# Optimization experiments

Hardware: AMD Instinct MI355X
Metric: run time of the kernel (lower is better)

Reference implementation:

```python
import jax, jax.numpy as jnp
import numpy as np

B, D, K = 8192, 1024, 30


def _sample_neg_indices(key, batch_size, num_negs):
    # per-row uniform indices in [0, 2B) excluding {i, i+B}, matching _sample_negatives
    total = 2 * batch_size
    i = jnp.arange(batch_size)[:, None]                      # [B,1]
    r = jax.random.randint(key, (batch_size, num_negs), 0, total - 2)
    a = r + (r >= i)                                         # skip index i
    b = a + (a >= (i + batch_size))                          # skip index i+B
    return b.astype(jnp.int32)


def setup_inputs() -> dict:
    key = jax.random.key(0)
    k1, k2, k3 = jax.random.split(key, 3)
    return {
        "z_i": jax.random.normal(k1, (B, D), dtype=jnp.float32),
        "z_j": jax.random.normal(k2, (B, D), dtype=jnp.float32),
        "temperature": jnp.asarray(0.2, dtype=jnp.float32),
        "neg_indices": _sample_neg_indices(k3, B, K),        # [B,K] int32
    }


def _l2_normalize(x, eps=1e-12):
    # matches F.normalize(p=2, dim=1): x / max(||x||, eps)
    n = jnp.sqrt(jnp.sum(x * x, axis=1, keepdims=True))
    return x / jnp.maximum(n, eps)


def reference(z_i, z_j, temperature, neg_indices):
    zi = _l2_normalize(z_i)                                  # [B,D]
    zj = _l2_normalize(z_j)                                  # [B,D]
    pos_sim = jnp.sum(zi * zj, axis=1)                       # [B]
    pool = jnp.concatenate([zi, zj], axis=0)                 # [2B,D]
    z_neg = pool[neg_indices]                                # [B,K,D] irregular gather
    neg_sim = jnp.einsum("bd,bkd->bk", zi, z_neg)            # [B,K]
    logits = jnp.concatenate([pos_sim[:, None], neg_sim], axis=1) / temperature  # [B,1+K]
    # cross entropy with labels == 0
    loss = -jnp.mean(jax.nn.log_softmax(logits, axis=1)[:, 0])
    return loss
```

## Files before the change

kernel.cpp:

```cpp
#include <hip/hip_runtime.h>
#include <math.h>

constexpr int NB = 8192;
constexpr int ND = 1024;
constexpr int NK = 30;
constexpr int RS = ND / 4;

#if defined(__has_builtin)
#  if __has_builtin(__builtin_amdgcn_sdot4)
#    define HAVE_SDOT4 1
#  endif
#endif
#ifndef HAVE_SDOT4
#  define HAVE_SDOT4 0
#endif

__device__ __forceinline__ int SDOT4(int a, int b, int acc) {
#if HAVE_SDOT4
    return __builtin_amdgcn_sdot4(a, b, acc, false);
#else
    return acc + (int)(signed char)(a)        * (int)(signed char)(b)
               + (int)(signed char)(a >> 8)   * (int)(signed char)(b >> 8)
               + (int)(signed char)(a >> 16)  * (int)(signed char)(b >> 16)
               + (int)(a >> 24)               * (int)(b >> 24);
#endif
}

__device__ __forceinline__ int pack4_i8(float a, float b, float c, float d) {
    int x0 = (int)rintf(a), x1 = (int)rintf(b), x2 = (int)rintf(c), x3 = (int)rintf(d);
    return (x0 & 255) | ((x1 & 255) << 8) | ((x2 & 255) << 16) | (x3 << 24);
}

__global__ void normalize_i8_kernel(const float* __restrict__ zi,
                                    const float* __restrict__ zj,
                                    int* __restrict__ pool,
                                    int* __restrict__ logits) {
    if (threadIdx.x < 64)
        logits[blockIdx.x * 64 + threadIdx.x] = 0;

    int row  = blockIdx.x * 4 + (threadIdx.x >> 6);
    int lane = threadIdx.x & 63;
    const float* src = (row < NB) ? (zi + (size_t)row * ND)
                                  : (zj + (size_t)(row - NB) * ND);
    float v[16];
    float s = 0.f;
#pragma unroll
    for (int seg = 0; seg < 4; ++seg) {
        float4 t = *reinterpret_cast<const float4*>(src + lane * 16 + seg * 4);
        v[seg * 4 + 0] = t.x; v[seg * 4 + 1] = t.y;
        v[seg * 4 + 2] = t.z; v[seg * 4 + 3] = t.w;
        s += t.x * t.x + t.y * t.y + t.z * t.z + t.w * t.w;
    }
#pragma unroll
    for (int off = 32; off >= 1; off >>= 1)
        s += __shfl_xor(s, off, 64);
    float inv = 127.f / fmaxf(sqrtf(s), 1e-12f);

    int4 w;
    w.x = pack4_i8(v[0]*inv,  v[1]*inv,  v[2]*inv,  v[3]*inv);
    w.y = pack4_i8(v[4]*inv,  v[5]*inv,  v[6]*inv,  v[7]*inv);
    w.z = pack4_i8(v[8]*inv,  v[9]*inv,  v[10]*inv, v[11]*inv);
    w.w = pack4_i8(v[12]*inv, v[13]*inv, v[14]*inv, v[15]*inv);
    *reinterpret_cast<int4*>(pool + (size_t)row * RS + lane * 4) = w;
}

__global__ void loss_chunk_kernel(const int* __restrict__ pool,
                                  const int* __restrict__ neg_idx,
                                  int* __restrict__ logits) {
    int wave = threadIdx.x >> 6;
    int lane = threadIdx.x & 63;
    int c    = blockIdx.x & 7;
    int row  = (blockIdx.x >> 3) * 4 + wave;
    int g    = lane >> 3;
    int p    = lane & 7;

    int myidx = (lane < NK) ? neg_idx[row * NK + lane] : 0;

    const int* cbase = pool + c * 32 + p * 4;
    int4 a4 = *reinterpret_cast<const int4*>(cbase + (size_t)row * RS);

    int4 b4[4];
#pragma unroll
    for (int t = 0; t < 4; ++t) {
        int s = t * 8 + g;
        int r = (s == 0) ? (row + NB)
              : (s < 31) ? __shfl(myidx, s - 1, 64)
                         : 0;
        b4[t] = *reinterpret_cast<const int4*>(cbase + (size_t)r * RS);
    }

    int d0 = 0, d1 = 0, d2 = 0, d3 = 0;
    d0 = SDOT4(a4.x, b4[0].x, d0); d0 = SDOT4(a4.y, b4[0].y, d0);
    d0 = SDOT4(a4.z, b4[0].z, d0); d0 = SDOT4(a4.w, b4[0].w, d0);
    d1 = SDOT4(a4.x, b4[1].x, d1); d1 = SDOT4(a4.y, b4[1].y, d1);
    d1 = SDOT4(a4.z, b4[1].z, d1); d1 = SDOT4(a4.w, b4[1].w, d1);
    d2 = SDOT4(a4.x, b4[2].x, d2); d2 = SDOT4(a4.y, b4[2].y, d2);
    d2 = SDOT4(a4.z, b4[2].z, d2); d2 = SDOT4(a4.w, b4[2].w, d2);
    d3 = SDOT4(a4.x, b4[3].x, d3); d3 = SDOT4(a4.y, b4[3].y, d3);
    d3 = SDOT4(a4.z, b4[3].z, d3); d3 = SDOT4(a4.w, b4[3].w, d3);

#pragma unroll
    for (int off = 1; off <= 4; off <<= 1) {
        d0 += __shfl_xor(d0, off, 64);
        d1 += __shfl_xor(d1, off, 64);
        d2 += __shfl_xor(d2, off, 64);
        d3 += __shfl_xor(d3, off, 64);
    }

    if (p < 4) {
        int val = (p == 0) ? d0 : (p == 1) ? d1 : (p == 2) ? d2 : d3;
        atomicAdd(&logits[row * 32 + p * 8 + g], val);
    }
}

__global__ void lse_kernel(const int* __restrict__ logits,
                           const float* __restrict__ temp_ptr,
                           float* __restrict__ block_part) {
    int wave = threadIdx.x >> 6;
    int lane = threadIdx.x & 63;
    int slot = lane & 31;
    int row  = blockIdx.x * 8 + wave * 2 + (lane >> 5);

    float inv_t = 1.f / (127.f * 127.f * temp_ptr[0]);

    float l = (slot < 31) ? logits[row * 32 + slot] * inv_t : -1e30f;

    float m = l;
#pragma unroll
    for (int off = 1; off <= 16; off <<= 1)
        m = fmaxf(m, __shfl_xor(m, off, 64));
    float e = __expf(l - m);
#pragma unroll
    for (int off = 1; off <= 16; off <<= 1)
        e += __shfl_xor(e, off, 64);

    float l0   = __shfl(l, lane & 32, 64);
    float loss = (m + logf(e)) - l0;
    float loss2 = __shfl(loss, 32, 64);

    __shared__ float red[4];
    if (lane == 0) red[wave] = loss + loss2;
    __syncthreads();
    if (threadIdx.x == 0)
        block_part[blockIdx.x] = red[0] + red[1] + red[2] + red[3];
}

__global__ void reduce_kernel(const float* __restrict__ partial, int n,
                              float* __restrict__ out) {
    float s = 0.f;
    for (int i = threadIdx.x; i < n; i += 256) s += partial[i];
#pragma unroll
    for (int off = 32; off >= 1; off >>= 1)
        s += __shfl_xor(s, off, 64);
    __shared__ float lds[4];
    int wave = threadIdx.x >> 6, lane = threadIdx.x & 63;
    if (lane == 0) lds[wave] = s;
    __syncthreads();
    if (threadIdx.x == 0)
        out[0] = (lds[0] + lds[1] + lds[2] + lds[3]) * (1.f / (float)NB);
}

__global__ void norms_kernel(const float* __restrict__ zi,
                             const float* __restrict__ zj,
                             float* __restrict__ inv_norm) {
    int row  = blockIdx.x * 4 + (threadIdx.x >> 6);
    int lane = threadIdx.x & 63;
    if (row >= 2 * NB) return;
    const float* src = (row < NB) ? (zi + (size_t)row * ND)
                                  : (zj + (size_t)(row - NB) * ND);
    float s = 0.f;
#pragma unroll
    for (int seg = 0; seg < 4; ++seg) {
        float4 v = *reinterpret_cast<const float4*>(src + seg * 256 + lane * 4);
        s += v.x*v.x + v.y*v.y + v.z*v.z + v.w*v.w;
    }
#pragma unroll
    for (int off = 32; off >= 1; off >>= 1)
        s += __shfl_xor(s, off, 64);
    if (lane == 0)
        inv_norm[row] = 1.f / fmaxf(sqrtf(s), 1e-12f);
}

__global__ void loss_kernel_f32(const float* __restrict__ zi,
                                const float* __restrict__ zj,
                                const int*   __restrict__ neg_idx,
                                const float* __restrict__ temp_ptr,
                                const float* __restrict__ inv_norm,
                                float* __restrict__ partial) {
    int wave = threadIdx.x >> 6;
    int lane = threadIdx.x & 63;
    int row  = blockIdx.x * 4 + wave;
    float inv_t = 1.f / temp_ptr[0];
    const float* a = zi + (size_t)row * ND;
    float4 av[4];
#pragma unroll
    for (int seg = 0; seg < 4; ++seg)
        av[seg] = *reinterpret_cast<const float4*>(a + seg * 256 + lane * 4);
    float inv_a = inv_norm[row];
    float m = -INFINITY, ssum = 0.f, logit0 = 0.f;
    for (int k = -1; k < NK; ++k) {
        int r = (k < 0) ? (row + NB) : neg_idx[row * NK + k];
        const float* bp = (r < NB) ? (zi + (size_t)r * ND)
                                   : (zj + (size_t)(r - NB) * ND);
        float inv_b = inv_norm[r];
        float dot = 0.f;
#pragma unroll
        for (int seg = 0; seg < 4; ++seg) {
            float4 bv = *reinterpret_cast<const float4*>(bp + seg * 256 + lane * 4);
            dot += av[seg].x*bv.x + av[seg].y*bv.y + av[seg].z*bv.z + av[seg].w*bv.w;
        }
#pragma unroll
        for (int off = 32; off >= 1; off >>= 1)
            dot += __shfl_xor(dot, off, 64);
        float logit = dot * inv_a * inv_b * inv_t;
        if (k < 0) logit0 = logit;
        if (logit > m) { ssum = ssum * __expf(m - logit) + 1.f; m = logit; }
        else           { ssum += __expf(logit - m); }
    }
    float loss = (m + logf(ssum)) - logit0;
    __shared__ float red[4];
    if (lane == 0) red[wave] = loss;
    __syncthreads();
    if (threadIdx.x == 0)
        partial[blockIdx.x] = red[0] + red[1] + red[2] + red[3];
}

extern "C" void kernel_launch(void* const* d_in, const int* in_sizes, int n_in,
                              void* d_out, int out_size, void* d_ws, size_t ws_size,
                              hipStream_t stream) {
    const float* zi      = (const float*)d_in[0];
    const float* zj      = (const float*)d_in[1];
    const float* temp    = (const float*)d_in[2];
    const int*   neg_idx = (const int*)d_in[3];
    float* out = (float*)d_out;

    const size_t pool_bytes   = (size_t)2 * NB * ND;
    const size_t logits_bytes = (size_t)NB * 32 * sizeof(int);
    const size_t block_bytes  = (size_t)(NB / 8) * sizeof(float);

    if (ws_size >= pool_bytes + logits_bytes + block_bytes) {
        int*   pool       = (int*)d_ws;
        int*   logits     = (int*)((char*)d_ws + pool_bytes);
        float* block_part = (float*)((char*)d_ws + pool_bytes + logits_bytes);

        normalize_i8_kernel<<<(2 * NB) / 4, 256, 0, stream>>>(zi, zj, pool, logits);
        loss_chunk_kernel<<<(NB / 4) * 8, 256, 0, stream>>>(pool, neg_idx, logits);
        lse_kernel<<<NB / 8, 256, 0, stream>>>(logits, temp, block_part);
        reduce_kernel<<<1, 256, 0, stream>>>(block_part, NB / 8, out);
    } else {
        float* inv_norm = (float*)d_ws;
        float* partial  = inv_norm + 2 * NB;

        norms_kernel<<<(2 * NB) / 4, 256, 0, stream>>>(zi, zj, inv_norm);
        loss_kernel_f32<<<NB / 4, 256, 0, stream>>>(zi, zj, neg_idx, temp,
                                                    inv_norm, partial);
        reduce_kernel<<<1, 256, 0, stream>>>(partial, NB / 4, out);
    }
}
```

Baseline: 40.34 us.

## Quantize pool to int4 with sdot8 and fold final reduction into atomics

Normalized embeddings are now packed as 4-bit signed values (scale 40, clamped to [-8,7]) and dot products use the sdot8 instruction when available. This halves the pool footprint and the bytes gathered per negative, and it halves the number of chunk blocks. The separate final reduce kernel is removed: the LSE blocks atomically add their scaled partial sums into the output, which is zeroed in the normalize kernel. The cost is a much coarser similarity approximation, which risks the loss drifting beyond tolerance, and an atomic-order-dependent float sum.

Measured after the change: 49.59 us. +22.9%, slower.

```diff
diff --git a/kernel.cpp b/kernel.cpp
--- a/kernel.cpp
+++ b/kernel.cpp
@@ -4,15 +4,34 @@
 constexpr int NB = 8192;
 constexpr int ND = 1024;
 constexpr int NK = 30;
-constexpr int RS = ND / 4;
 
 #if defined(__has_builtin)
+#  if __has_builtin(__builtin_amdgcn_sdot8)
+#    define HAVE_SDOT8 1
+#  endif
 #  if __has_builtin(__builtin_amdgcn_sdot4)
 #    define HAVE_SDOT4 1
 #  endif
 #endif
+#ifndef HAVE_SDOT8
+#  define HAVE_SDOT8 0
+#endif
 #ifndef HAVE_SDOT4
 #  define HAVE_SDOT4 0
+#endif
+
+#if HAVE_SDOT8
+constexpr int   RSI    = 128;
+constexpr int   CMASK  = 3;
+constexpr int   CSH    = 2;
+constexpr float SCALE  = 40.f;
+constexpr float SCALE2 = 1600.f;
+#else
+constexpr int   RSI    = 256;
+constexpr int   CMASK  = 7;
+constexpr int   CSH    = 3;
+constexpr float SCALE  = 127.f;
+constexpr float SCALE2 = 16129.f;
 #endif
 
 __device__ __forceinline__ int SDOT4(int a, int b, int acc) {
@@ -26,15 +45,42 @@
 #endif
 }
 
+__device__ __forceinline__ int DOT16(const int4& a, const int4& b, int acc) {
+#if HAVE_SDOT8
+    acc = __builtin_amdgcn_sdot8(a.x, b.x, acc, false);
+    acc = __builtin_amdgcn_sdot8(a.y, b.y, acc, false);
+    acc = __builtin_amdgcn_sdot8(a.z, b.z, acc, false);
+    acc = __builtin_amdgcn_sdot8(a.w, b.w, acc, false);
+#else
+    acc = SDOT4(a.x, b.x, acc);
+    acc = SDOT4(a.y, b.y, acc);
+    acc = SDOT4(a.z, b.z, acc);
+    acc = SDOT4(a.w, b.w, acc);
+#endif
+    return acc;
+}
+
 __device__ __forceinline__ int pack4_i8(float a, float b, float c, float d) {
     int x0 = (int)rintf(a), x1 = (int)rintf(b), x2 = (int)rintf(c), x3 = (int)rintf(d);
     return (x0 & 255) | ((x1 & 255) << 8) | ((x2 & 255) << 16) | (x3 << 24);
 }
 
-__global__ void normalize_i8_kernel(const float* __restrict__ zi,
-                                    const float* __restrict__ zj,
-                                    int* __restrict__ pool,
-                                    int* __restrict__ logits) {
+__device__ __forceinline__ int pack8_i4(const float* v, float s) {
+    int w = 0;
+#pragma unroll
+    for (int k = 0; k < 8; ++k) {
+        int q = (int)rintf(fminf(7.f, fmaxf(-8.f, v[k] * s)));
+        w |= (q & 0xF) << (4 * k);
+    }
+    return w;
+}
+
+__global__ void normalize_kernel(const float* __restrict__ zi,
+                                 const float* __restrict__ zj,
+                                 int* __restrict__ pool,
+                                 int* __restrict__ logits,
+                                 float* __restrict__ out) {
+    if (blockIdx.x == 0 && threadIdx.x == 0) out[0] = 0.f;
     if (threadIdx.x < 64)
         logits[blockIdx.x * 64 + threadIdx.x] = 0;
 
@@ -54,14 +100,21 @@
 #pragma unroll
     for (int off = 32; off >= 1; off >>= 1)
         s += __shfl_xor(s, off, 64);
-    float inv = 127.f / fmaxf(sqrtf(s), 1e-12f);
-
+    float inv = SCALE / fmaxf(sqrtf(s), 1e-12f);
+
+#if HAVE_SDOT8
+    int2 w;
+    w.x = pack8_i4(v, inv);
+    w.y = pack8_i4(v + 8, inv);
+    *reinterpret_cast<int2*>(pool + (size_t)row * RSI + lane * 2) = w;
+#else
     int4 w;
     w.x = pack4_i8(v[0]*inv,  v[1]*inv,  v[2]*inv,  v[3]*inv);
     w.y = pack4_i8(v[4]*inv,  v[5]*inv,  v[6]*inv,  v[7]*inv);
     w.z = pack4_i8(v[8]*inv,  v[9]*inv,  v[10]*inv, v[11]*inv);
     w.w = pack4_i8(v[12]*inv, v[13]*inv, v[14]*inv, v[15]*inv);
-    *reinterpret_cast<int4*>(pool + (size_t)row * RS + lane * 4) = w;
+    *reinterpret_cast<int4*>(pool + (size_t)row * RSI + lane * 4) = w;
+#endif
 }
 
 __global__ void loss_chunk_kernel(const int* __restrict__ pool,
@@ -69,15 +122,15 @@
                                   int* __restrict__ logits) {
     int wave = threadIdx.x >> 6;
     int lane = threadIdx.x & 63;
-    int c    = blockIdx.x & 7;
-    int row  = (blockIdx.x >> 3) * 4 + wave;
+    int c    = blockIdx.x & CMASK;
+    int row  = (blockIdx.x >> CSH) * 4 + wave;
     int g    = lane >> 3;
     int p    = lane & 7;
 
     int myidx = (lane < NK) ? neg_idx[row * NK + lane] : 0;
 
     const int* cbase = pool + c * 32 + p * 4;
-    int4 a4 = *reinterpret_cast<const int4*>(cbase + (size_t)row * RS);
+    int4 a4 = *reinterpret_cast<const int4*>(cbase + (size_t)row * RSI);
 
     int4 b4[4];
 #pragma unroll
@@ -86,18 +139,14 @@
         int r = (s == 0) ? (row + NB)
               : (s < 31) ? __shfl(myidx, s - 1, 64)
                          : 0;
-        b4[t] = *reinterpret_cast<const int4*>(cbase + (size_t)r * RS);
+        b4[t] = *reinterpret_cast<const int4*>(cbase + (size_t)r * RSI);
     }
 
     int d0 = 0, d1 = 0, d2 = 0, d3 = 0;
-    d0 = SDOT4(a4.x, b4[0].x, d0); d0 = SDOT4(a4.y, b4[0].y, d0);
-    d0 = SDOT4(a4.z, b4[0].z, d0); d0 = SDOT4(a4.w, b4[0].w, d0);
-    d1 = SDOT4(a4.x, b4[1].x, d1); d1 = SDOT4(a4.y, b4[1].y, d1);
-    d1 = SDOT4(a4.z, b4[1].z, d1); d1 = SDOT4(a4.w, b4[1].w, d1);
-    d2 = SDOT4(a4.x, b4[2].x, d2); d2 = SDOT4(a4.y, b4[2].y, d2);
-    d2 = SDOT4(a4.z, b4[2].z, d2); d2 = SDOT4(a4.w, b4[2].w, d2);
-    d3 = SDOT4(a4.x, b4[3].x, d3); d3 = SDOT4(a4.y, b4[3].y, d3);
-    d3 = SDOT4(a4.z, b4[3].z, d3); d3 = SDOT4(a4.w, b4[3].w, d3);
+    d0 = DOT16(a4, b4[0], d0);
+    d1 = DOT16(a4, b4[1], d1);
+    d2 = DOT16(a4, b4[2], d2);
+    d3 = DOT16(a4, b4[3], d3);
 
 #pragma unroll
     for (int off = 1; off <= 4; off <<= 1) {
@@ -115,13 +164,13 @@
 
 __global__ void lse_kernel(const int* __restrict__ logits,
                            const float* __restrict__ temp_ptr,
-                           float* __restrict__ block_part) {
+                           float* __restrict__ out) {
     int wave = threadIdx.x >> 6;
     int lane = threadIdx.x & 63;
     int slot = lane & 31;
     int row  = blockIdx.x * 8 + wave * 2 + (lane >> 5);
 
-    float inv_t = 1.f / (127.f * 127.f * temp_ptr[0]);
+    float inv_t = 1.f / (SCALE2 * temp_ptr[0]);
 
     float l = (slot < 31) ? logits[row * 32 + slot] * inv_t : -1e30f;
 
@@ -134,30 +183,15 @@
     for (int off = 1; off <= 16; off <<= 1)
         e += __shfl_xor(e, off, 64);
 
-    float l0   = __shfl(l, lane & 32, 64);
-    float loss = (m + logf(e)) - l0;
+    float l0    = __shfl(l, lane & 32, 64);
+    float loss  = (m + logf(e)) - l0;
     float loss2 = __shfl(loss, 32, 64);
 
     __shared__ float red[4];
     if (lane == 0) red[wave] = loss + loss2;
     __syncthreads();
     if (threadIdx.x == 0)
-        block_part[blockIdx.x] = red[0] + red[1] + red[2] + red[3];
-}
-
-__global__ void reduce_kernel(const float* __restrict__ partial, int n,
-                              float* __restrict__ out) {
-    float s = 0.f;
-    for (int i = threadIdx.x; i < n; i += 256) s += partial[i];
-#pragma unroll
-    for (int off = 32; off >= 1; off >>= 1)
-        s += __shfl_xor(s, off, 64);
-    __shared__ float lds[4];
-    int wave = threadIdx.x >> 6, lane = threadIdx.x & 63;
-    if (lane == 0) lds[wave] = s;
-    __syncthreads();
-    if (threadIdx.x == 0)
-        out[0] = (lds[0] + lds[1] + lds[2] + lds[3]) * (1.f / (float)NB);
+        atomicAdd(out, (red[0] + red[1] + red[2] + red[3]) * (1.f / (float)NB));
 }
 
 __global__ void norms_kernel(const float* __restrict__ zi,
@@ -225,6 +259,21 @@
         partial[blockIdx.x] = red[0] + red[1] + red[2] + red[3];
 }
 
+__global__ void reduce_kernel(const float* __restrict__ partial, int n,
+                              float* __restrict__ out) {
+    float s = 0.f;
+    for (int i = threadIdx.x; i < n; i += 256) s += partial[i];
+#pragma unroll
+    for (int off = 32; off >= 1; off >>= 1)
+        s += __shfl_xor(s, off, 64);
+    __shared__ float lds[4];
+    int wave = threadIdx.x >> 6, lane = threadIdx.x & 63;
+    if (lane == 0) lds[wave] = s;
+    __syncthreads();
+    if (threadIdx.x == 0)
+        out[0] = (lds[0] + lds[1] + lds[2] + lds[3]) * (1.f / (float)NB);
+}
+
 extern "C" void kernel_launch(void* const* d_in, const int* in_sizes, int n_in,
                               void* d_out, int out_size, void* d_ws, size_t ws_size,
                               hipStream_t stream) {
@@ -234,19 +283,16 @@
     const int*   neg_idx = (const int*)d_in[3];
     float* out = (float*)d_out;
 
-    const size_t pool_bytes   = (size_t)2 * NB * ND;
+    const size_t pool_bytes   = (size_t)2 * NB * RSI * sizeof(int);
     const size_t logits_bytes = (size_t)NB * 32 * sizeof(int);
-    const size_t block_bytes  = (size_t)(NB / 8) * sizeof(float);
-
-    if (ws_size >= pool_bytes + logits_bytes + block_bytes) {
-        int*   pool       = (int*)d_ws;
-        int*   logits     = (int*)((char*)d_ws + pool_bytes);
-        float* block_part = (float*)((char*)d_ws + pool_bytes + logits_bytes);
-
-        normalize_i8_kernel<<<(2 * NB) / 4, 256, 0, stream>>>(zi, zj, pool, logits);
-        loss_chunk_kernel<<<(NB / 4) * 8, 256, 0, stream>>>(pool, neg_idx, logits);
-        lse_kernel<<<NB / 8, 256, 0, stream>>>(logits, temp, block_part);
-        reduce_kernel<<<1, 256, 0, stream>>>(block_part, NB / 8, out);
+
+    if (ws_size >= pool_bytes + logits_bytes) {
+        int* pool   = (int*)d_ws;
+        int* logits = (int*)((char*)d_ws + pool_bytes);
+
+        normalize_kernel<<<(2 * NB) / 4, 256, 0, stream>>>(zi, zj, pool, logits, out);
+        loss_chunk_kernel<<<(NB / 4) * (CMASK + 1), 256, 0, stream>>>(pool, neg_idx, logits);
+        lse_kernel<<<NB / 8, 256, 0, stream>>>(logits, temp, out);
     } else {
         float* inv_norm = (float*)d_ws;
         float* partial  = inv_norm + 2 * NB;
```
